# Kernel optimization log

Hardware: AMD Instinct MI355X
Metric: run time of the kernel (lower is better)

## Reference

```python
import jax, jax.numpy as jnp
import numpy as np

EPSILON = 0.1
MAX_ITER = 100
EPS_DIV = 1e-8

B, N, M = 1024, 256, 256


def setup_inputs() -> dict:
    key = jax.random.key(0)
    k1, k2, k3 = jax.random.split(key, 3)
    cost_matrix = jax.random.uniform(k1, (B, N, M), dtype=jnp.float32)
    mass_pred = jax.random.uniform(k2, (B, N), dtype=jnp.float32)
    mass_target = jax.random.uniform(k3, (B, M), dtype=jnp.float32)
    return {"cost_matrix": cost_matrix, "mass_pred": mass_pred, "mass_target": mass_target}


def reference(cost_matrix, mass_pred, mass_target):
    # normalize masses to probability distributions
    a = mass_pred / (mass_pred.sum(axis=-1, keepdims=True) + EPS_DIV)   # [B,N]
    b = mass_target / (mass_target.sum(axis=-1, keepdims=True) + EPS_DIV)  # [B,M]

    K = jnp.exp(-cost_matrix / EPSILON)  # [B,N,M]

    u0 = jnp.ones_like(a)
    v0 = jnp.ones_like(b)

    def step(carry, _):
        u, v = carry
        Kt_u = jnp.einsum('bnm,bn->bm', K, u)  # K^T u
        v = b / (Kt_u + EPS_DIV)
        K_v = jnp.einsum('bnm,bm->bn', K, v)   # K v
        u = a / (K_v + EPS_DIV)
        return (u, v), None

    (u, v), _ = jax.lax.scan(step, (u0, v0), None, length=MAX_ITER)

    P = u[:, :, None] * K * v[:, None, :]  # transport plan [B,N,M]
    ot_cost = jnp.sum(P * cost_matrix, axis=(-2, -1))  # [B]
    return ot_cost.mean()
```

## Files before the change

kernel.cpp:

```cpp
#include <hip/hip_runtime.h>

#define TPB 1024

#define SMEM_BYTES 134272

typedef _Float16 f16x8 __attribute__((ext_vector_type(8)));
typedef _Float16 f16x4 __attribute__((ext_vector_type(4)));
typedef _Float16 h2    __attribute__((ext_vector_type(2)));
typedef float    f32x4 __attribute__((ext_vector_type(4)));

union HU { unsigned u; h2 h; };

static __device__ __forceinline__ float sel4(f32x4 a, int c) {
    float x01 = (c & 1) ? a[1] : a[0];
    float x23 = (c & 1) ? a[3] : a[2];
    return (c & 2) ? x23 : x01;
}

__global__ __launch_bounds__(TPB, 4) void sinkhorn_kernel(
    const float* __restrict__ cost,
    const float* __restrict__ mass_pred,
    const float* __restrict__ mass_target,
    float* __restrict__ out)
{
    extern __shared__ char smem[];
    _Float16* Ksh = (_Float16*)smem;
    _Float16* uh  = (_Float16*)(smem + 131072);
    _Float16* vh  = (_Float16*)(smem + 131584);
    float* a_sh   = (float*)(smem + 132096);
    float* b_sh   = (float*)(smem + 133120);
    float* scr    = (float*)(smem + 134144);

    const int t    = threadIdx.x;
    const int bat  = blockIdx.x;
    const int l    = t & 63;
    const int w    = t >> 6;
    const int quad = (l >> 4) & 3;
    const int col  = l & 15;
    const int own  = 16 * w + 4 * quad + (col & 3);

    float vmp = 0.f, vmt = 0.f;
    if (t < 256) {
        vmp = mass_pred [bat * 256 + t];
        vmt = mass_target[bat * 256 + t];
    }
    float s1 = vmp, s2 = vmt;
#pragma unroll
    for (int o = 32; o > 0; o >>= 1) {
        s1 += __shfl_xor(s1, o);
        s2 += __shfl_xor(s2, o);
    }
    if (t < 256 && l == 0) { scr[w] = s1; scr[8 + w] = s2; }
    if (t < 256) uh[t] = (_Float16)1.0f;
    __syncthreads();
    if (t == 0) {
        float ta = 0.f, tb = 0.f;
#pragma unroll
        for (int ww = 0; ww < 4; ++ww) { ta += scr[ww]; tb += scr[8 + ww]; }
        scr[16] = ta + 1e-8f;
        scr[17] = tb + 1e-8f;
    }
    __syncthreads();
    if (t < 256) {
        a_sh[t] = vmp / scr[16];
        b_sh[t] = vmt / scr[17];
    }

    {
        const float4* C4 = (const float4*)(cost + (size_t)bat * 65536);
#pragma unroll 4
        for (int i = 0; i < 16; ++i) {
            int idx = i * TPB + t;
            float4 c = C4[idx];
            int n = idx >> 6, col4 = idx & 63;
            HU p01, p23;
            p01.h = (h2){(_Float16)__expf(c.x * -10.0f), (_Float16)__expf(c.y * -10.0f)};
            p23.h = (h2){(_Float16)__expf(c.z * -10.0f), (_Float16)__expf(c.w * -10.0f)};
            *(uint2*)((char*)Ksh + n * 512 + col4 * 8) = make_uint2(p01.u, p23.u);
        }
    }
    __syncthreads();

    f16x8 afrag[8];
#pragma unroll
    for (int c = 0; c < 8; ++c) {
#pragma unroll
        for (int j = 0; j < 8; ++j)
            afrag[c][j] = Ksh[(32 * c + quad * 8 + j) * 256 + 16 * w + col];
    }
    f16x8 bfrag[8];
#pragma unroll
    for (int c = 0; c < 8; ++c)
        bfrag[c] = *(const f16x8*)&Ksh[(16 * w + col) * 256 + 32 * c + quad * 8];

    for (int it = 0; it < 100; ++it) {
        {
            float bb = b_sh[own];
            f16x8 uf0 = *(const f16x8*)&uh[quad * 8];
            f16x8 uf1 = *(const f16x8*)&uh[32 + quad * 8];
            f16x8 uf2 = *(const f16x8*)&uh[64 + quad * 8];
            f16x8 uf3 = *(const f16x8*)&uh[96 + quad * 8];
            f16x8 uf4 = *(const f16x8*)&uh[128 + quad * 8];
            f16x8 uf5 = *(const f16x8*)&uh[160 + quad * 8];
            f16x8 uf6 = *(const f16x8*)&uh[192 + quad * 8];
            f16x8 uf7 = *(const f16x8*)&uh[224 + quad * 8];
            f32x4 c0 = {0.f, 0.f, 0.f, 0.f}, c1 = c0, c2 = c0, c3 = c0;
            c0 = __builtin_amdgcn_mfma_f32_16x16x32_f16(afrag[0], uf0, c0, 0, 0, 0);
            c1 = __builtin_amdgcn_mfma_f32_16x16x32_f16(afrag[1], uf1, c1, 0, 0, 0);
            c2 = __builtin_amdgcn_mfma_f32_16x16x32_f16(afrag[2], uf2, c2, 0, 0, 0);
            c3 = __builtin_amdgcn_mfma_f32_16x16x32_f16(afrag[3], uf3, c3, 0, 0, 0);
            c0 = __builtin_amdgcn_mfma_f32_16x16x32_f16(afrag[4], uf4, c0, 0, 0, 0);
            c1 = __builtin_amdgcn_mfma_f32_16x16x32_f16(afrag[5], uf5, c1, 0, 0, 0);
            c2 = __builtin_amdgcn_mfma_f32_16x16x32_f16(afrag[6], uf6, c2, 0, 0, 0);
            c3 = __builtin_amdgcn_mfma_f32_16x16x32_f16(afrag[7], uf7, c3, 0, 0, 0);
            float kt = (sel4(c0, col) + sel4(c1, col)) +
                       (sel4(c2, col) + sel4(c3, col));
            float vvv = bb * __builtin_amdgcn_rcpf(kt + 1e-8f);
            if (col < 4) vh[own] = (_Float16)vvv;
        }
        __syncthreads();

        {
            float aa = a_sh[own];
            f16x8 vf0 = *(const f16x8*)&vh[quad * 8];
            f16x8 vf1 = *(const f16x8*)&vh[32 + quad * 8];
            f16x8 vf2 = *(const f16x8*)&vh[64 + quad * 8];
            f16x8 vf3 = *(const f16x8*)&vh[96 + quad * 8];
            f16x8 vf4 = *(const f16x8*)&vh[128 + quad * 8];
            f16x8 vf5 = *(const f16x8*)&vh[160 + quad * 8];
            f16x8 vf6 = *(const f16x8*)&vh[192 + quad * 8];
            f16x8 vf7 = *(const f16x8*)&vh[224 + quad * 8];
            f32x4 c0 = {0.f, 0.f, 0.f, 0.f}, c1 = c0, c2 = c0, c3 = c0;
            c0 = __builtin_amdgcn_mfma_f32_16x16x32_f16(bfrag[0], vf0, c0, 0, 0, 0);
            c1 = __builtin_amdgcn_mfma_f32_16x16x32_f16(bfrag[1], vf1, c1, 0, 0, 0);
            c2 = __builtin_amdgcn_mfma_f32_16x16x32_f16(bfrag[2], vf2, c2, 0, 0, 0);
            c3 = __builtin_amdgcn_mfma_f32_16x16x32_f16(bfrag[3], vf3, c3, 0, 0, 0);
            c0 = __builtin_amdgcn_mfma_f32_16x16x32_f16(bfrag[4], vf4, c0, 0, 0, 0);
            c1 = __builtin_amdgcn_mfma_f32_16x16x32_f16(bfrag[5], vf5, c1, 0, 0, 0);
            c2 = __builtin_amdgcn_mfma_f32_16x16x32_f16(bfrag[6], vf6, c2, 0, 0, 0);
            c3 = __builtin_amdgcn_mfma_f32_16x16x32_f16(bfrag[7], vf7, c3, 0, 0, 0);
            float kv = (sel4(c0, col) + sel4(c1, col)) +
                       (sel4(c2, col) + sel4(c3, col));
            float uuu = aa * __builtin_amdgcn_rcpf(kv + 1e-8f);
            if (col < 4) uh[own] = (_Float16)uuu;
        }
        __syncthreads();
    }

    float s = 0.f;
    {
        float uN = (float)uh[16 * w + col];
#pragma unroll
        for (int c = 0; c < 8; ++c) {
            f16x8 vf = *(const f16x8*)&vh[32 * c + quad * 8];
#pragma unroll
            for (int j = 0; j < 8; ++j) {
                float kv = (float)bfrag[c][j];
                float cv = -0.1f * __logf(kv);
                s = fmaf(kv * cv, (float)vf[j], s);
            }
        }
        s *= uN;
    }
#pragma unroll
    for (int o = 32; o > 0; o >>= 1) s += __shfl_xor(s, o);
    if (l == 0) scr[w] = s;
    __syncthreads();
    if (t == 0) {
        float tot = 0.f;
#pragma unroll
        for (int ww = 0; ww < 16; ++ww) tot += scr[ww];
        atomicAdd(out, tot * (1.0f / 1024.0f));
    }
}

extern "C" void kernel_launch(void* const* d_in, const int* in_sizes, int n_in,
                              void* d_out, int out_size, void* d_ws, size_t ws_size,
                              hipStream_t stream) {
    const float* cost = (const float*)d_in[0];
    const float* mp   = (const float*)d_in[1];
    const float* mt   = (const float*)d_in[2];
    float* out = (float*)d_out;

    hipMemsetAsync(out, 0, sizeof(float), stream);

    hipFuncSetAttribute((const void*)sinkhorn_kernel,
                        hipFuncAttributeMaxDynamicSharedMemorySize, SMEM_BYTES);

    sinkhorn_kernel<<<1024, TPB, SMEM_BYTES, stream>>>(cost, mp, mt, out);
}
```

Measured before the change: 702.2 us.

## Replace block barriers with LDS flag-based pairwise signaling and double-buffered u

```diff
diff --git a/kernel.cpp b/kernel.cpp
--- a/kernel.cpp
+++ b/kernel.cpp
@@ -2,7 +2,7 @@
 
 #define TPB 1024
 
-#define SMEM_BYTES 134272
+#define SMEM_BYTES 134848
 
 typedef _Float16 f16x8 __attribute__((ext_vector_type(8)));
 typedef _Float16 f16x4 __attribute__((ext_vector_type(4)));
@@ -15,6 +15,23 @@
     float x01 = (c & 1) ? a[1] : a[0];
     float x23 = (c & 1) ? a[3] : a[2];
     return (c & 2) ? x23 : x01;
+}
+
+#define SPIN_MAX 4096
+static __device__ __forceinline__ void wait4(const int* f, int lim) {
+    for (int k = 0; k < SPIN_MAX; ++k) {
+        int f0 = __hip_atomic_load(&f[0], __ATOMIC_RELAXED, __HIP_MEMORY_SCOPE_WORKGROUP);
+        int f1 = __hip_atomic_load(&f[1], __ATOMIC_RELAXED, __HIP_MEMORY_SCOPE_WORKGROUP);
+        int f2 = __hip_atomic_load(&f[2], __ATOMIC_RELAXED, __HIP_MEMORY_SCOPE_WORKGROUP);
+        int f3 = __hip_atomic_load(&f[3], __ATOMIC_RELAXED, __HIP_MEMORY_SCOPE_WORKGROUP);
+        if (f0 >= lim && f1 >= lim && f2 >= lim && f3 >= lim) break;
+    }
+    __builtin_amdgcn_fence(__ATOMIC_ACQUIRE, "workgroup");
+}
+
+static __device__ __forceinline__ void signal(int* f) {
+    __builtin_amdgcn_fence(__ATOMIC_RELEASE, "workgroup");
+    __hip_atomic_fetch_add(f, 1, __ATOMIC_RELAXED, __HIP_MEMORY_SCOPE_WORKGROUP);
 }
 
 __global__ __launch_bounds__(TPB, 4) void sinkhorn_kernel(
@@ -25,11 +42,14 @@
 {
     extern __shared__ char smem[];
     _Float16* Ksh = (_Float16*)smem;
-    _Float16* uh  = (_Float16*)(smem + 131072);
-    _Float16* vh  = (_Float16*)(smem + 131584);
-    float* a_sh   = (float*)(smem + 132096);
-    float* b_sh   = (float*)(smem + 133120);
-    float* scr    = (float*)(smem + 134144);
+    _Float16* u0  = (_Float16*)(smem + 131072);
+    _Float16* u1  = (_Float16*)(smem + 131584);
+    _Float16* vh  = (_Float16*)(smem + 132096);
+    float* a_sh   = (float*)(smem + 132608);
+    float* b_sh   = (float*)(smem + 133632);
+    float* scr    = (float*)(smem + 134656);
+    int*   aflag  = (int*)(smem + 134784);
+    int*   bflag  = (int*)(smem + 134816);
 
     const int t    = threadIdx.x;
     const int bat  = blockIdx.x;
@@ -38,7 +58,9 @@
     const int quad = (l >> 4) & 3;
     const int col  = l & 15;
     const int own  = 16 * w + 4 * quad + (col & 3);
-
+    const int pair = w >> 1;
+
+    if (t < 8) { aflag[t] = 0; bflag[t] = 0; }
     float vmp = 0.f, vmt = 0.f;
     if (t < 256) {
         vmp = mass_pred [bat * 256 + t];
@@ -51,7 +73,7 @@
         s2 += __shfl_xor(s2, o);
     }
     if (t < 256 && l == 0) { scr[w] = s1; scr[8 + w] = s2; }
-    if (t < 256) uh[t] = (_Float16)1.0f;
+    if (t < 256) u0[t] = (_Float16)1.0f;
     __syncthreads();
     if (t == 0) {
         float ta = 0.f, tb = 0.f;
@@ -93,22 +115,30 @@
     for (int c = 0; c < 8; ++c)
         bfrag[c] = *(const f16x8*)&Ksh[(16 * w + col) * 256 + 32 * c + quad * 8];
 
+    const float bb = b_sh[own];
+    const float aa = a_sh[own];
+
+    _Float16* ucur = u0;
+    _Float16* unxt = u1;
     for (int it = 0; it < 100; ++it) {
+        const int limB = 2 * it;
+        const int limA = 2 * it + 2;
         {
-            float bb = b_sh[own];
-            f16x8 uf0 = *(const f16x8*)&uh[quad * 8];
-            f16x8 uf1 = *(const f16x8*)&uh[32 + quad * 8];
-            f16x8 uf2 = *(const f16x8*)&uh[64 + quad * 8];
-            f16x8 uf3 = *(const f16x8*)&uh[96 + quad * 8];
-            f16x8 uf4 = *(const f16x8*)&uh[128 + quad * 8];
-            f16x8 uf5 = *(const f16x8*)&uh[160 + quad * 8];
-            f16x8 uf6 = *(const f16x8*)&uh[192 + quad * 8];
-            f16x8 uf7 = *(const f16x8*)&uh[224 + quad * 8];
             f32x4 c0 = {0.f, 0.f, 0.f, 0.f}, c1 = c0, c2 = c0, c3 = c0;
+            wait4(&bflag[0], limB);
+            f16x8 uf0 = *(const f16x8*)&ucur[quad * 8];
+            f16x8 uf1 = *(const f16x8*)&ucur[32 + quad * 8];
+            f16x8 uf2 = *(const f16x8*)&ucur[64 + quad * 8];
+            f16x8 uf3 = *(const f16x8*)&ucur[96 + quad * 8];
             c0 = __builtin_amdgcn_mfma_f32_16x16x32_f16(afrag[0], uf0, c0, 0, 0, 0);
             c1 = __builtin_amdgcn_mfma_f32_16x16x32_f16(afrag[1], uf1, c1, 0, 0, 0);
             c2 = __builtin_amdgcn_mfma_f32_16x16x32_f16(afrag[2], uf2, c2, 0, 0, 0);
             c3 = __builtin_amdgcn_mfma_f32_16x16x32_f16(afrag[3], uf3, c3, 0, 0, 0);
+            wait4(&bflag[4], limB);
+            f16x8 uf4 = *(const f16x8*)&ucur[128 + quad * 8];
+            f16x8 uf5 = *(const f16x8*)&ucur[160 + quad * 8];
+            f16x8 uf6 = *(const f16x8*)&ucur[192 + quad * 8];
+            f16x8 uf7 = *(const f16x8*)&ucur[224 + quad * 8];
             c0 = __builtin_amdgcn_mfma_f32_16x16x32_f16(afrag[4], uf4, c0, 0, 0, 0);
             c1 = __builtin_amdgcn_mfma_f32_16x16x32_f16(afrag[5], uf5, c1, 0, 0, 0);
             c2 = __builtin_amdgcn_mfma_f32_16x16x32_f16(afrag[6], uf6, c2, 0, 0, 0);
@@ -117,24 +147,25 @@
                        (sel4(c2, col) + sel4(c3, col));
             float vvv = bb * __builtin_amdgcn_rcpf(kt + 1e-8f);
             if (col < 4) vh[own] = (_Float16)vvv;
-        }
-        __syncthreads();
+            if (l == 0) signal(&aflag[pair]);
+        }
 
         {
-            float aa = a_sh[own];
+            f32x4 c0 = {0.f, 0.f, 0.f, 0.f}, c1 = c0, c2 = c0, c3 = c0;
+            wait4(&aflag[0], limA);
             f16x8 vf0 = *(const f16x8*)&vh[quad * 8];
             f16x8 vf1 = *(const f16x8*)&vh[32 + quad * 8];
             f16x8 vf2 = *(const f16x8*)&vh[64 + quad * 8];
             f16x8 vf3 = *(const f16x8*)&vh[96 + quad * 8];
+            c0 = __builtin_amdgcn_mfma_f32_16x16x32_f16(bfrag[0], vf0, c0, 0, 0, 0);
+            c1 = __builtin_amdgcn_mfma_f32_16x16x32_f16(bfrag[1], vf1, c1, 0, 0, 0);
+            c2 = __builtin_amdgcn_mfma_f32_16x16x32_f16(bfrag[2], vf2, c2, 0, 0, 0);
+            c3 = __builtin_amdgcn_mfma_f32_16x16x32_f16(bfrag[3], vf3, c3, 0, 0, 0);
+            wait4(&aflag[4], limA);
             f16x8 vf4 = *(const f16x8*)&vh[128 + quad * 8];
             f16x8 vf5 = *(const f16x8*)&vh[160 + quad * 8];
             f16x8 vf6 = *(const f16x8*)&vh[192 + quad * 8];
             f16x8 vf7 = *(const f16x8*)&vh[224 + quad * 8];
-            f32x4 c0 = {0.f, 0.f, 0.f, 0.f}, c1 = c0, c2 = c0, c3 = c0;
-            c0 = __builtin_amdgcn_mfma_f32_16x16x32_f16(bfrag[0], vf0, c0, 0, 0, 0);
-            c1 = __builtin_amdgcn_mfma_f32_16x16x32_f16(bfrag[1], vf1, c1, 0, 0, 0);
-            c2 = __builtin_amdgcn_mfma_f32_16x16x32_f16(bfrag[2], vf2, c2, 0, 0, 0);
-            c3 = __builtin_amdgcn_mfma_f32_16x16x32_f16(bfrag[3], vf3, c3, 0, 0, 0);
             c0 = __builtin_amdgcn_mfma_f32_16x16x32_f16(bfrag[4], vf4, c0, 0, 0, 0);
             c1 = __builtin_amdgcn_mfma_f32_16x16x32_f16(bfrag[5], vf5, c1, 0, 0, 0);
             c2 = __builtin_amdgcn_mfma_f32_16x16x32_f16(bfrag[6], vf6, c2, 0, 0, 0);
@@ -142,14 +173,16 @@
             float kv = (sel4(c0, col) + sel4(c1, col)) +
                        (sel4(c2, col) + sel4(c3, col));
             float uuu = aa * __builtin_amdgcn_rcpf(kv + 1e-8f);
-            if (col < 4) uh[own] = (_Float16)uuu;
-        }
-        __syncthreads();
-    }
+            if (col < 4) unxt[own] = (_Float16)uuu;
+            if (l == 0) signal(&bflag[pair]);
+        }
+        _Float16* tmp = ucur; ucur = unxt; unxt = tmp;
+    }
+    __syncthreads();
 
     float s = 0.f;
     {
-        float uN = (float)uh[16 * w + col];
+        float uN = (float)ucur[16 * w + col];
 #pragma unroll
         for (int c = 0; c < 8; ++c) {
             f16x8 vf = *(const f16x8*)&vh[32 * c + quad * 8];
```

Result: slower. 865.2 us (+23.2%).
